# Kernel tuning notes

Measured on AMD Instinct MI355X. Metric: run time of the kernel, lower is better.

## Reference

```python
import jax, jax.numpy as jnp
import numpy as np

B, N, C_IN, G = 8, 65536, 16, 64
CH = [16, 16]
EPS = 1e-3  # keras BatchNormalization default epsilon
OFFSETS = [(dx, dy, dz) for dx in (-1, 0, 1) for dy in (-1, 0, 1) for dz in (-1, 0, 1)]
G3 = G * G * G


def setup_inputs() -> dict:
    key = jax.random.key(0)
    k = jax.random.split(key, 8)
    voxel_features = jax.random.normal(k[0], (B, N, C_IN), dtype=jnp.float32)
    # unique active voxel coordinates per example (submanifold sites)
    lin = jax.vmap(lambda kk: jax.random.permutation(kk, G3)[:N])(jax.random.split(k[1], B))
    xyz = jnp.stack([lin // (G * G), (lin // G) % G, lin % G], axis=-1).astype(jnp.int32)
    num_valid_voxels = jax.random.randint(k[2], (B,), N // 2, N + 1).astype(jnp.int32)
    w0 = jax.random.uniform(k[3], (3, 3, 3, C_IN, CH[0]), minval=-0.05, maxval=0.05, dtype=jnp.float32)
    w1 = jax.random.uniform(k[4], (3, 3, 3, CH[0], CH[1]), minval=-0.05, maxval=0.05, dtype=jnp.float32)
    nw0 = jax.random.uniform(k[5], (3, 3, 3, 1, 1), minval=-0.05, maxval=0.05, dtype=jnp.float32)
    nw1 = jax.random.uniform(k[6], (3, 3, 3, 1, 1), minval=-0.05, maxval=0.05, dtype=jnp.float32)
    gamma0 = jnp.ones((CH[0],), jnp.float32); beta0 = jnp.zeros((CH[0],), jnp.float32)
    gamma1 = jnp.ones((CH[1],), jnp.float32); beta1 = jnp.zeros((CH[1],), jnp.float32)
    return dict(voxel_features=voxel_features, voxel_xyz_indices=xyz,
                num_valid_voxels=num_valid_voxels, w0=w0, w1=w1, nw0=nw0, nw1=nw1,
                gamma0=gamma0, beta0=beta0, gamma1=gamma1, beta1=beta1)


def build_neighbor_idx(coords, valid_mask):
    """For each voxel and each 3x3x3 offset, the row index of the active neighbor, or -1."""
    lin = coords[..., 0] * (G * G) + coords[..., 1] * G + coords[..., 2]  # [B,N]
    # invalid (padded) voxels write to a spare slot so they never match as neighbors
    write_lin = jnp.where(valid_mask, lin, G3 + 1)
    idx_map = jnp.full((B, G3 + 2), -1, jnp.int32)
    idx_map = idx_map.at[jnp.arange(B)[:, None], write_lin].set(
        jnp.broadcast_to(jnp.arange(N, dtype=jnp.int32)[None, :], (B, N)))
    brow = jnp.arange(B)[:, None]
    nb = []
    for dx, dy, dz in OFFSETS:
        nx = coords[..., 0] + dx; ny = coords[..., 1] + dy; nz = coords[..., 2] + dz
        inb = (nx >= 0) & (nx < G) & (ny >= 0) & (ny < G) & (nz >= 0) & (nz < G)
        nlin = jnp.where(inb, nx * (G * G) + ny * G + nz, G3)  # slot G3 always -1
        nb.append(idx_map[brow, nlin])
    return jnp.stack(nb, axis=1)  # [B,27,N]


def sparse_conv(feats, nb_idx, valid_mask, w):
    """Submanifold sparse 3D conv: output only at active sites, gathering active neighbors."""
    wf = w.reshape(27, w.shape[3], w.shape[4])  # offsets enumerate kernel taps in order
    out = jnp.zeros((feats.shape[0], feats.shape[1], w.shape[4]), feats.dtype)
    for o in range(27):
        idx = nb_idx[:, o]  # [B,N]
        g = jnp.take_along_axis(feats, jnp.maximum(idx, 0)[..., None], axis=1)
        g = jnp.where((idx >= 0)[..., None], g, 0.0)
        out = out + jnp.einsum('bnc,co->bno', g, wf[o])
    return out * valid_mask[..., None]


def masked_bn(x, valid_mask, num_valid, gamma, beta):
    m = valid_mask[..., None].astype(x.dtype)
    cnt = jnp.sum(num_valid).astype(x.dtype)
    mean = jnp.sum(x * m, axis=(0, 1)) / cnt
    var = jnp.sum(m * jnp.square(x - mean), axis=(0, 1)) / cnt
    xn = (x - mean) * jax.lax.rsqrt(var + EPS) * gamma + beta
    return xn * m  # padded rows are zero-padded, as in the TF layer


def reference(voxel_features, voxel_xyz_indices, num_valid_voxels,
              w0, w1, nw0, nw1, gamma0, beta0, gamma1, beta1):
    valid_mask = jnp.arange(N)[None, :] < num_valid_voxels[:, None]  # [B,N]
    nb_idx = build_neighbor_idx(voxel_xyz_indices, valid_mask)
    ones = jnp.ones((B, N, 1), jnp.float32)
    net = voxel_features
    for w, nw, g, b in ((w0, nw0, gamma0, beta0), (w1, nw1, gamma1, beta1)):
        net = sparse_conv(net, nb_idx, valid_mask, w)
        net_norm = sparse_conv(ones, nb_idx, valid_mask, nw)
        net = net / (1.0 + jnp.abs(net_norm))
        net = masked_bn(net, valid_mask, num_valid_voxels, g, b)
        net = jax.nn.relu(net)
    return net
```

## Files before the change

### kernel.cpp

```cpp
#include <hip/hip_runtime.h>
#include <cstdint>
#include <cstddef>

#define NB 8
#define NN 65536
#define NS (NN + 16)
#define GG 64
#define GG3 (GG*GG*GG)
#define NW (GG3/32)
#define NBLKC 2048
#define NP32 (NB * 2048)
#define EPSC 1e-3f

typedef __bf16 bf16x8 __attribute__((ext_vector_type(8)));
typedef float  f32x4  __attribute__((ext_vector_type(4)));

__device__ __forceinline__ unsigned short f2bf(float f) {
    unsigned u = __builtin_bit_cast(unsigned, f);
    unsigned r = (u + 0x7fffu + ((u >> 16) & 1u)) >> 16;
    return (unsigned short)r;
}
__device__ __forceinline__ unsigned pk2(float a, float b) {
    return (unsigned)f2bf(a) | ((unsigned)f2bf(b) << 16);
}
__device__ __forceinline__ float bf2f(unsigned short s) {
    return __builtin_bit_cast(float, (unsigned)s << 16);
}

__device__ __forceinline__ int site_rank2(const int2* __restrict__ mwb, int lin) {
    int2 mw = mwb[lin >> 5];
    uint32_t w = (uint32_t)mw.x;
    uint32_t bit = 1u << (lin & 31);
    if (!(w & bit)) return -1;
    return mw.y + __popc(w & (bit - 1u));
}

__global__ __launch_bounds__(256) void build_mask_kernel(
    const int* __restrict__ xyz, const int* __restrict__ nvv,
    uint32_t* __restrict__ mask, int* __restrict__ linb,
    const float* __restrict__ w0, const float* __restrict__ w1,
    unsigned short* __restrict__ wf)
{
    int b = blockIdx.y;
    int n = blockIdx.x * 256 + threadIdx.x;
    if (n < nvv[b]) {
        const int* cp = xyz + ((size_t)b * NN + n) * 3;
        int lin = cp[0] * (GG * GG) + cp[1] * GG + cp[2];
        linb[(size_t)b * NN + n] = lin;
        atomicOr(&mask[b * NW + (lin >> 5)], 1u << (lin & 31));
    }
    if (blockIdx.x == 0 && b < 2) {
        const float* w = b ? w1 : w0;
        unsigned short* o = wf + b * 14 * 512;
        for (int idx = threadIdx.x; idx < 14 * 512; idx += 256) {
            int i = idx >> 9;
            int rem = idx & 511;
            int L = rem >> 3, j = rem & 7;
            int quad = L >> 4, nn = L & 15;
            int off = 2 * i + (quad >> 1);
            int c = ((quad & 1) << 3) + j;
            float v = (off < 27) ? w[(off * 16 + c) * 16 + nn] : 0.f;
            o[idx] = f2bf(v);
        }
    }
}

__global__ __launch_bounds__(256) void scan_mask_kernel(
    const uint32_t* __restrict__ mask, int2* __restrict__ mwb)
{
    int b = blockIdx.x;
    const uint32_t* mb = mask + (size_t)b * NW;
    int2* wb = mwb + (size_t)b * NW;
    int t = threadIdx.x;

    uint32_t wv[32];
    int cnts[32];
    int local = 0;
    #pragma unroll
    for (int i = 0; i < 32; i++) {
        wv[i] = mb[t * 32 + i];
        cnts[i] = __popc(wv[i]);
        local += cnts[i];
    }

    __shared__ int sc[256];
    sc[t] = local;
    __syncthreads();
    for (int off = 1; off < 256; off <<= 1) {
        int v = (t >= off) ? sc[t - off] : 0;
        __syncthreads();
        sc[t] += v;
        __syncthreads();
    }
    int base = sc[t] - local;
    #pragma unroll
    for (int i = 0; i < 32; i++) {
        wb[t * 32 + i] = make_int2((int)wv[i], base);
        base += cnts[i];
    }
}

__global__ __launch_bounds__(256) void perm_gather_kernel(
    const int* __restrict__ linb, const int* __restrict__ nvv,
    const int2* __restrict__ mwb,
    const float* __restrict__ feats,
    int2* __restrict__ srow,
    unsigned short* __restrict__ sfeats)
{
    int b = blockIdx.y;
    int n = blockIdx.x * 256 + threadIdx.x;
    int cnt = nvv[b];
    unsigned short* sfb = sfeats + (size_t)b * NS * 16;
    if (blockIdx.x == 0 && threadIdx.x < 16)
        sfb[(size_t)NN * 16 + threadIdx.x] = 0;
    if (n < cnt) {
        int lin = linb[(size_t)b * NN + n];
        int r = site_rank2(mwb + (size_t)b * NW, lin);
        srow[(size_t)b * NN + r] = make_int2(lin, n);
        const float4* fp = (const float4*)(feats + ((size_t)b * NN + n) * 16);
        float4 f0 = fp[0], f1 = fp[1], f2 = fp[2], f3 = fp[3];
        uint4 lo = make_uint4(pk2(f0.x, f0.y), pk2(f0.z, f0.w),
                              pk2(f1.x, f1.y), pk2(f1.z, f1.w));
        uint4 hi = make_uint4(pk2(f2.x, f2.y), pk2(f2.z, f2.w),
                              pk2(f3.x, f3.y), pk2(f3.z, f3.w));
        *(uint4*)(sfb + (size_t)r * 16)     = lo;
        *(uint4*)(sfb + (size_t)r * 16 + 8) = hi;
    }
}

__global__ __launch_bounds__(256, 4) void conv_mfma_kernel(
    const unsigned short* __restrict__ sfeats,
    const int2*     __restrict__ srow,
    const int*      __restrict__ nvv,
    const int2*     __restrict__ mwb,
    const unsigned short* __restrict__ wfrag,
    const float*    __restrict__ nw,
    unsigned short* __restrict__ outbuf,
    float*          __restrict__ stats)
{
    int lane = threadIdx.x & 63;
    int wv = threadIdx.x >> 6;
    int m = lane & 15, quad = lane >> 4;
    int v = lane & 31, h = lane >> 5;
    int wid = blockIdx.x * 4 + wv;

    __shared__ int   ubuf[4][32 * 29];
    __shared__ float rrl[4][32];
    __shared__ float red[4][32];
    __shared__ float lnw[27];
    int*   jj   = ubuf[wv];
    float* obuf = (float*)ubuf[wv];

    if (threadIdx.x < 27) lnw[threadIdx.x] = nw[threadIdx.x];

    bf16x8 bfr[14];
    #pragma unroll
    for (int i = 0; i < 14; i++)
        bfr[i] = *(const bf16x8*)(wfrag + i * 512 + lane * 8);
    __syncthreads();

    float psum = 0.f, psq = 0.f;
    int coff = (quad & 1) << 3;

    for (int pb = wid; pb < NP32; pb += 4 * NBLKC) {
        int b = pb >> 11;
        int r0 = (pb & 2047) << 5;
        int cnt = nvv[b];
        if (r0 >= cnt) continue;

        const int2* mb = mwb + (size_t)b * NW;
        const unsigned short* fb = sfeats + (size_t)b * NS * 16;
        const int2* sr = srow + (size_t)b * NN;

        int Rv = r0 + v;
        bool vld = Rv < cnt;
        int lin = vld ? sr[Rv].x : 0;
        int x = lin >> 12, y = (lin >> 6) & 63, z = lin & 63;
        int zb = z & 31;
        float nc = 0.f;
        #pragma unroll
        for (int t = 0; t < 5; t++) {
            int c = 2 * t + h;
            bool cok = c < 9;
            int cc = cok ? c : 0;
            int dx = cc / 3 - 1, dy = cc % 3 - 1;
            int nx = x + dx, ny = y + dy;
            bool colok = cok & ((unsigned)nx < 64u) & ((unsigned)ny < 64u);
            int wdi = colok ? (((nx << 12) + (ny << 6) + z) >> 5) : 0;

            int2 mw = make_int2(0, 0);
            if (vld & colok) mw = mb[wdi];
            bool need2 = vld & colok & (((zb == 0) & (z > 0)) | ((zb == 31) & (z < 63)));
            int w2 = wdi + ((zb == 0) ? -1 : 1);
            int2 mw2 = make_int2(0, 0);
            if (need2) mw2 = mb[w2];

            #pragma unroll
            for (int dz = -1; dz <= 1; dz++) {
                int zz = z + dz;
                bool zok = (unsigned)zz < 64u;
                bool same = (dz == 0) | ((dz < 0) ? (zb != 0) : (zb != 31));
                int2 word = same ? mw : mw2;
                int bb = zz & 31;
                uint32_t wm = (uint32_t)word.x;
                bool hit = vld & colok & zok & ((wm >> bb) & 1u);
                int rnk = word.y + __popc(wm & ((1u << bb) - 1u));
                int off = cc * 3 + dz + 1;
                int jv = hit ? rnk : NN;
                if (cok) {
                    jj[v * 29 + off] = jv;
                    nc += hit ? lnw[off] : 0.f;
                }
            }
        }
        nc += __shfl_xor(nc, 32, 64);
        if (lane < 32) rrl[wv][v] = 1.f / (1.f + fabsf(nc));

        f32x4 acc0 = {0.f, 0.f, 0.f, 0.f};
        f32x4 acc1 = {0.f, 0.f, 0.f, 0.f};
        #pragma unroll
        for (int i = 0; i < 14; i++) {
            int off = 2 * i + (quad >> 1);
            int idx = off < 27 ? off : 28;
            int j0 = jj[m * 29 + idx];        j0 = (off < 27) ? j0 : NN;
            int j1 = jj[(m + 16) * 29 + idx]; j1 = (off < 27) ? j1 : NN;
            bf16x8 a0 = *(const bf16x8*)(fb + (size_t)j0 * 16 + coff);
            bf16x8 a1 = *(const bf16x8*)(fb + (size_t)j1 * 16 + coff);
            acc0 = __builtin_amdgcn_mfma_f32_16x16x32_bf16(a0, bfr[i], acc0, 0, 0, 0);
            acc1 = __builtin_amdgcn_mfma_f32_16x16x32_bf16(a1, bfr[i], acc1, 0, 0, 0);
        }

        #pragma unroll
        for (int hh = 0; hh < 2; hh++) {
            #pragma unroll
            for (int r4 = 0; r4 < 4; r4++) {
                int row = (hh << 4) + (quad << 2) + r4;
                float tval = (hh ? acc1[r4] : acc0[r4]) * rrl[wv][row];
                psum += tval; psq += tval * tval;
                obuf[row * 17 + m] = tval;
            }
        }
        {
            int Rr = r0 + v;
            if (Rr < cnt) {
                const float* src = &obuf[v * 17 + h * 8];
                uint4 val = make_uint4(pk2(src[0], src[1]), pk2(src[2], src[3]),
                                       pk2(src[4], src[5]), pk2(src[6], src[7]));
                *(uint4*)(outbuf + ((size_t)b * NS + Rr) * 16 + h * 8) = val;
            }
        }
    }

    psum += __shfl_xor(psum, 16, 64); psum += __shfl_xor(psum, 32, 64);
    psq  += __shfl_xor(psq, 16, 64);  psq  += __shfl_xor(psq, 32, 64);
    if (lane < 16) { red[wv][lane] = psum; red[wv][16 + lane] = psq; }
    __syncthreads();
    if (threadIdx.x < 32) {
        float vv = red[0][threadIdx.x] + red[1][threadIdx.x] +
                   red[2][threadIdx.x] + red[3][threadIdx.x];
        atomicAdd(&stats[(blockIdx.x & 15) * 32 + threadIdx.x], vv);
    }
}

__device__ __forceinline__ void compute_sb(
    const float* __restrict__ stats, const int* __restrict__ nvv,
    const float* __restrict__ gamma, const float* __restrict__ beta,
    float* sbs , float* sums )
{
    int tid = threadIdx.x;
    if (tid < 32) {
        float v = 0.f;
        #pragma unroll
        for (int s = 0; s < 16; s++) v += stats[s * 32 + tid];
        sums[tid] = v;
    }
    __syncthreads();
    if (tid < 16) {
        float cnt = 0.f;
        #pragma unroll
        for (int b = 0; b < NB; b++) cnt += (float)nvv[b];
        float mean = sums[tid] / cnt;
        float var  = fmaxf(sums[16 + tid] / cnt - mean * mean, 0.f);
        float scv = gamma[tid] * rsqrtf(var + EPSC);
        sbs[tid]      = scv;
        sbs[16 + tid] = beta[tid] - mean * scv;
    }
    __syncthreads();
}

__global__ __launch_bounds__(256) void bnrelu_sorted_kernel(
    unsigned short* __restrict__ buf, const float* __restrict__ stats,
    const int* __restrict__ nvv,
    const float* __restrict__ gamma, const float* __restrict__ beta)
{
    __shared__ float sbs[32];
    __shared__ float sums[32];
    compute_sb(stats, nvv, gamma, beta, sbs, sums);

    int b = blockIdx.y;
    int r = blockIdx.x * 256 + threadIdx.x;
    if (r > NN) return;
    int cnt = nvv[b];
    unsigned short* op = buf + ((size_t)b * NS + r) * 16;
    if (r < cnt) {
        uint4 xl = *(const uint4*)op, xh = *(const uint4*)(op + 8);
        float y[16];
        #pragma unroll
        for (int c = 0; c < 16; c++) {
            unsigned u = (c < 8) ? ((const unsigned*)&xl)[c >> 1]
                                 : ((const unsigned*)&xh)[(c - 8) >> 1];
            unsigned short sv = (c & 1) ? (unsigned short)(u >> 16)
                                        : (unsigned short)(u & 0xffff);
            y[c] = fmaxf(fmaf(bf2f(sv), sbs[c], sbs[16 + c]), 0.f);
        }
        *(uint4*)op       = make_uint4(pk2(y[0], y[1]), pk2(y[2], y[3]),
                                       pk2(y[4], y[5]), pk2(y[6], y[7]));
        *(uint4*)(op + 8) = make_uint4(pk2(y[8], y[9]), pk2(y[10], y[11]),
                                       pk2(y[12], y[13]), pk2(y[14], y[15]));
    } else if (r == NN) {
        uint4 z = make_uint4(0, 0, 0, 0);
        *(uint4*)op       = z;
        *(uint4*)(op + 8) = z;
    }
}

__global__ __launch_bounds__(256) void final_scatter_kernel(
    const unsigned short* __restrict__ in,
    const int2* __restrict__ srow,
    const float* __restrict__ stats, const int* __restrict__ nvv,
    const float* __restrict__ gamma, const float* __restrict__ beta,
    float* __restrict__ out)
{
    __shared__ float sbs[32];
    __shared__ float sums[32];
    compute_sb(stats, nvv, gamma, beta, sbs, sums);

    int b = blockIdx.y;
    int r = blockIdx.x * 256 + threadIdx.x;
    int cnt = nvv[b];
    if (r < cnt) {
        const uint4* ip = (const uint4*)(in + ((size_t)b * NS + r) * 16);
        uint4 xl = ip[0], xh = ip[1];
        float y[16];
        #pragma unroll
        for (int c = 0; c < 16; c++) {
            unsigned u = (c < 8) ? ((const unsigned*)&xl)[c >> 1]
                                 : ((const unsigned*)&xh)[(c - 8) >> 1];
            unsigned short sv = (c & 1) ? (unsigned short)(u >> 16)
                                        : (unsigned short)(u & 0xffff);
            y[c] = fmaxf(fmaf(bf2f(sv), sbs[c], sbs[16 + c]), 0.f);
        }
        int n = srow[(size_t)b * NN + r].y;
        float4* op = (float4*)(out + ((size_t)b * NN + n) * 16);
        op[0] = make_float4(y[0],  y[1],  y[2],  y[3]);
        op[1] = make_float4(y[4],  y[5],  y[6],  y[7]);
        op[2] = make_float4(y[8],  y[9],  y[10], y[11]);
        op[3] = make_float4(y[12], y[13], y[14], y[15]);
    } else {
        float4 z = make_float4(0.f, 0.f, 0.f, 0.f);
        float4* op = (float4*)(out + ((size_t)b * NN + r) * 16);
        op[0] = z; op[1] = z; op[2] = z; op[3] = z;
    }
}

extern "C" void kernel_launch(void* const* d_in, const int* in_sizes, int n_in,
                              void* d_out, int out_size, void* d_ws, size_t ws_size,
                              hipStream_t stream)
{
    const float* feats  = (const float*)d_in[0];
    const int*   xyz    = (const int*)d_in[1];
    const int*   nvv    = (const int*)d_in[2];
    const float* w0     = (const float*)d_in[3];
    const float* w1     = (const float*)d_in[4];
    const float* nw0    = (const float*)d_in[5];
    const float* nw1    = (const float*)d_in[6];
    const float* gamma0 = (const float*)d_in[7];
    const float* beta0  = (const float*)d_in[8];
    const float* gamma1 = (const float*)d_in[9];
    const float* beta1  = (const float*)d_in[10];
    float* out = (float*)d_out;

    char* ws = (char*)d_ws;
    uint32_t* mask    = (uint32_t*)ws;       ws += (size_t)NB * NW * 4;
    float*    stats1  = (float*)ws;          ws += 16 * 32 * 4;
    float*    stats2  = (float*)ws;          ws += 16 * 32 * 4;
    int2*     mwb     = (int2*)ws;           ws += (size_t)NB * NW * 8;
    int2*     srow    = (int2*)ws;           ws += (size_t)NB * NN * 8;
    int*      linb    = (int*)ws;            ws += (size_t)NB * NN * 4;
    unsigned short* sfA = (unsigned short*)ws; ws += (size_t)NB * NS * 16 * 2;
    unsigned short* sfB = (unsigned short*)ws; ws += (size_t)NB * NS * 16 * 2;
    unsigned short* wfr = (unsigned short*)ws; ws += (size_t)2 * 14 * 512 * 2;

    hipMemsetAsync(mask, 0, (size_t)NB * NW * 4 + 16 * 32 * 4 * 2, stream);

    dim3 gridBN(NN / 256, NB);
    build_mask_kernel<<<gridBN, 256, 0, stream>>>(xyz, nvv, mask, linb, w0, w1, wfr);
    scan_mask_kernel<<<NB, 256, 0, stream>>>(mask, mwb);
    perm_gather_kernel<<<gridBN, 256, 0, stream>>>(linb, nvv, mwb, feats, srow, sfA);

    conv_mfma_kernel<<<NBLKC, 256, 0, stream>>>(
        sfA, srow, nvv, mwb, wfr, nw0, sfB, stats1);
    bnrelu_sorted_kernel<<<dim3(NN / 256 + 1, NB), 256, 0, stream>>>(
        sfB, stats1, nvv, gamma0, beta0);

    conv_mfma_kernel<<<NBLKC, 256, 0, stream>>>(
        sfB, srow, nvv, mwb, wfr + 14 * 512, nw1, sfA, stats2);

    final_scatter_kernel<<<dim3(NN / 256, NB), 256, 0, stream>>>(
        sfA, srow, stats2, nvv, gamma1, beta1, out);
}
```

Measured before the change: 242.0 us.

## Fuse first BN+ReLU into second conv gather and make final output a gather

Removes the standalone BN/ReLU pass over the sorted intermediate by applying the scale/bias and ReLU to each gathered neighbor row inside the second convolution, masking the sentinel zero row explicitly. The sorted-row table is split into a linear-coordinate array and an original-to-sorted index map, so the final kernel reads via gather and writes output coalesced instead of scattering. This trades a full memory pass and a launch for redundant per-neighbor ALU work (27x per row) in the conv inner loop.

Result: slower. 275.5 us (+13.8%).

```diff
diff --git a/kernel.cpp b/kernel.cpp
--- a/kernel.cpp
+++ b/kernel.cpp
@@ -104,7 +104,7 @@
     const int* __restrict__ linb, const int* __restrict__ nvv,
     const int2* __restrict__ mwb,
     const float* __restrict__ feats,
-    int2* __restrict__ srow,
+    int* __restrict__ slin, int* __restrict__ n2r,
     unsigned short* __restrict__ sfeats)
 {
     int b = blockIdx.y;
@@ -116,7 +116,8 @@
     if (n < cnt) {
         int lin = linb[(size_t)b * NN + n];
         int r = site_rank2(mwb + (size_t)b * NW, lin);
-        srow[(size_t)b * NN + r] = make_int2(lin, n);
+        slin[(size_t)b * NN + r] = lin;
+        n2r[(size_t)b * NN + n] = r;
         const float4* fp = (const float4*)(feats + ((size_t)b * NN + n) * 16);
         float4 f0 = fp[0], f1 = fp[1], f2 = fp[2], f3 = fp[3];
         uint4 lo = make_uint4(pk2(f0.x, f0.y), pk2(f0.z, f0.w),
@@ -128,13 +129,43 @@
     }
 }
 
+__device__ __forceinline__ void compute_sb(
+    const float* __restrict__ stats, const int* __restrict__ nvv,
+    const float* __restrict__ gamma, const float* __restrict__ beta,
+    float* sbs , float* sums )
+{
+    int tid = threadIdx.x;
+    if (tid < 32) {
+        float v = 0.f;
+        #pragma unroll
+        for (int s = 0; s < 16; s++) v += stats[s * 32 + tid];
+        sums[tid] = v;
+    }
+    __syncthreads();
+    if (tid < 16) {
+        float cnt = 0.f;
+        #pragma unroll
+        for (int b = 0; b < NB; b++) cnt += (float)nvv[b];
+        float mean = sums[tid] / cnt;
+        float var  = fmaxf(sums[16 + tid] / cnt - mean * mean, 0.f);
+        float scv = gamma[tid] * rsqrtf(var + EPSC);
+        sbs[tid]      = scv;
+        sbs[16 + tid] = beta[tid] - mean * scv;
+    }
+    __syncthreads();
+}
+
+template<bool FUSEBN>
 __global__ __launch_bounds__(256, 4) void conv_mfma_kernel(
     const unsigned short* __restrict__ sfeats,
-    const int2*     __restrict__ srow,
+    const int*      __restrict__ slin,
     const int*      __restrict__ nvv,
     const int2*     __restrict__ mwb,
     const unsigned short* __restrict__ wfrag,
     const float*    __restrict__ nw,
+    const float*    __restrict__ statsin,
+    const float*    __restrict__ gammain,
+    const float*    __restrict__ betain,
     unsigned short* __restrict__ outbuf,
     float*          __restrict__ stats)
 {
@@ -148,10 +179,23 @@
     __shared__ float rrl[4][32];
     __shared__ float red[4][32];
     __shared__ float lnw[27];
+    __shared__ float sbs[32];
+    __shared__ float sums[32];
     int*   jj   = ubuf[wv];
     float* obuf = (float*)ubuf[wv];
 
     if (threadIdx.x < 27) lnw[threadIdx.x] = nw[threadIdx.x];
+    if (FUSEBN) compute_sb(statsin, nvv, gammain, betain, sbs, sums);
+
+    int coff = (quad & 1) << 3;
+    float sc8[8], bi8[8];
+    if (FUSEBN) {
+        #pragma unroll
+        for (int k = 0; k < 8; k++) {
+            sc8[k] = sbs[coff + k];
+            bi8[k] = sbs[16 + coff + k];
+        }
+    }
 
     bf16x8 bfr[14];
     #pragma unroll
@@ -160,7 +204,6 @@
     __syncthreads();
 
     float psum = 0.f, psq = 0.f;
-    int coff = (quad & 1) << 3;
 
     for (int pb = wid; pb < NP32; pb += 4 * NBLKC) {
         int b = pb >> 11;
@@ -170,11 +213,11 @@
 
         const int2* mb = mwb + (size_t)b * NW;
         const unsigned short* fb = sfeats + (size_t)b * NS * 16;
-        const int2* sr = srow + (size_t)b * NN;
+        const int* sr = slin + (size_t)b * NN;
 
         int Rv = r0 + v;
         bool vld = Rv < cnt;
-        int lin = vld ? sr[Rv].x : 0;
+        int lin = vld ? sr[Rv] : 0;
         int x = lin >> 12, y = (lin >> 6) & 63, z = lin & 63;
         int zb = z & 31;
         float nc = 0.f;
@@ -226,6 +269,22 @@
             int j1 = jj[(m + 16) * 29 + idx]; j1 = (off < 27) ? j1 : NN;
             bf16x8 a0 = *(const bf16x8*)(fb + (size_t)j0 * 16 + coff);
             bf16x8 a1 = *(const bf16x8*)(fb + (size_t)j1 * 16 + coff);
+            if (FUSEBN) {
+                bf16x8 t0, t1;
+                #pragma unroll
+                for (int k = 0; k < 8; k++) {
+                    float y0 = fmaxf(fmaf((float)a0[k], sc8[k], bi8[k]), 0.f);
+                    float y1 = fmaxf(fmaf((float)a1[k], sc8[k], bi8[k]), 0.f);
+                    t0[k] = (__bf16)y0;
+                    t1[k] = (__bf16)y1;
+                }
+                uint4 u0 = __builtin_bit_cast(uint4, t0);
+                uint4 u1 = __builtin_bit_cast(uint4, t1);
+                if (j0 == NN) { u0 = make_uint4(0, 0, 0, 0); }
+                if (j1 == NN) { u1 = make_uint4(0, 0, 0, 0); }
+                a0 = __builtin_bit_cast(bf16x8, u0);
+                a1 = __builtin_bit_cast(bf16x8, u1);
+            }
             acc0 = __builtin_amdgcn_mfma_f32_16x16x32_bf16(a0, bfr[i], acc0, 0, 0, 0);
             acc1 = __builtin_amdgcn_mfma_f32_16x16x32_bf16(a1, bfr[i], acc1, 0, 0, 0);
         }
@@ -262,48 +321,25 @@
     }
 }
 
-__device__ __forceinline__ void compute_sb(
+__global__ __launch_bounds__(256) void final_gather_kernel(
+    const unsigned short* __restrict__ in,
+    const int* __restrict__ n2r,
     const float* __restrict__ stats, const int* __restrict__ nvv,
     const float* __restrict__ gamma, const float* __restrict__ beta,
-    float* sbs , float* sums )
-{
-    int tid = threadIdx.x;
-    if (tid < 32) {
-        float v = 0.f;
-        #pragma unroll
-        for (int s = 0; s < 16; s++) v += stats[s * 32 + tid];
-        sums[tid] = v;
-    }
-    __syncthreads();
-    if (tid < 16) {
-        float cnt = 0.f;
-        #pragma unroll
-        for (int b = 0; b < NB; b++) cnt += (float)nvv[b];
-        float mean = sums[tid] / cnt;
-        float var  = fmaxf(sums[16 + tid] / cnt - mean * mean, 0.f);
-        float scv = gamma[tid] * rsqrtf(var + EPSC);
-        sbs[tid]      = scv;
-        sbs[16 + tid] = beta[tid] - mean * scv;
-    }
-    __syncthreads();
-}
-
-__global__ __launch_bounds__(256) void bnrelu_sorted_kernel(
-    unsigned short* __restrict__ buf, const float* __restrict__ stats,
-    const int* __restrict__ nvv,
-    const float* __restrict__ gamma, const float* __restrict__ beta)
+    float* __restrict__ out)
 {
     __shared__ float sbs[32];
     __shared__ float sums[32];
     compute_sb(stats, nvv, gamma, beta, sbs, sums);
 
     int b = blockIdx.y;
-    int r = blockIdx.x * 256 + threadIdx.x;
-    if (r > NN) return;
+    int n = blockIdx.x * 256 + threadIdx.x;
     int cnt = nvv[b];
-    unsigned short* op = buf + ((size_t)b * NS + r) * 16;
-    if (r < cnt) {
-        uint4 xl = *(const uint4*)op, xh = *(const uint4*)(op + 8);
+    float4* op = (float4*)(out + ((size_t)b * NN + n) * 16);
+    if (n < cnt) {
+        int r = n2r[(size_t)b * NN + n];
+        const uint4* ip = (const uint4*)(in + ((size_t)b * NS + r) * 16);
+        uint4 xl = ip[0], xh = ip[1];
         float y[16];
         #pragma unroll
         for (int c = 0; c < 16; c++) {
@@ -313,52 +349,12 @@
                                         : (unsigned short)(u & 0xffff);
             y[c] = fmaxf(fmaf(bf2f(sv), sbs[c], sbs[16 + c]), 0.f);
         }
-        *(uint4*)op       = make_uint4(pk2(y[0], y[1]), pk2(y[2], y[3]),
-                                       pk2(y[4], y[5]), pk2(y[6], y[7]));
-        *(uint4*)(op + 8) = make_uint4(pk2(y[8], y[9]), pk2(y[10], y[11]),
-                                       pk2(y[12], y[13]), pk2(y[14], y[15]));
-    } else if (r == NN) {
-        uint4 z = make_uint4(0, 0, 0, 0);
-        *(uint4*)op       = z;
-        *(uint4*)(op + 8) = z;
-    }
-}
-
-__global__ __launch_bounds__(256) void final_scatter_kernel(
-    const unsigned short* __restrict__ in,
-    const int2* __restrict__ srow,
-    const float* __restrict__ stats, const int* __restrict__ nvv,
-    const float* __restrict__ gamma, const float* __restrict__ beta,
-    float* __restrict__ out)
-{
-    __shared__ float sbs[32];
-    __shared__ float sums[32];
-    compute_sb(stats, nvv, gamma, beta, sbs, sums);
-
-    int b = blockIdx.y;
-    int r = blockIdx.x * 256 + threadIdx.x;
-    int cnt = nvv[b];
-    if (r < cnt) {
-        const uint4* ip = (const uint4*)(in + ((size_t)b * NS + r) * 16);
-        uint4 xl = ip[0], xh = ip[1];
-        float y[16];
-        #pragma unroll
-        for (int c = 0; c < 16; c++) {
-            unsigned u = (c < 8) ? ((const unsigned*)&xl)[c >> 1]
-                                 : ((const unsigned*)&xh)[(c - 8) >> 1];
-            unsigned short sv = (c & 1) ? (unsigned short)(u >> 16)
-                                        : (unsigned short)(u & 0xffff);
-            y[c] = fmaxf(fmaf(bf2f(sv), sbs[c], sbs[16 + c]), 0.f);
-        }
-        int n = srow[(size_t)b * NN + r].y;
-        float4* op = (float4*)(out + ((size_t)b * NN + n) * 16);
         op[0] = make_float4(y[0],  y[1],  y[2],  y[3]);
         op[1] = make_float4(y[4],  y[5],  y[6],  y[7]);
         op[2] = make_float4(y[8],  y[9],  y[10], y[11]);
         op[3] = make_float4(y[12], y[13], y[14], y[15]);
     } else {
         float4 z = make_float4(0.f, 0.f, 0.f, 0.f);
-        float4* op = (float4*)(out + ((size_t)b * NN + r) * 16);
         op[0] = z; op[1] = z; op[2] = z; op[3] = z;
     }
 }
@@ -385,7 +381,8 @@
     float*    stats1  = (float*)ws;          ws += 16 * 32 * 4;
     float*    stats2  = (float*)ws;          ws += 16 * 32 * 4;
     int2*     mwb     = (int2*)ws;           ws += (size_t)NB * NW * 8;
-    int2*     srow    = (int2*)ws;           ws += (size_t)NB * NN * 8;
+    int*      slin    = (int*)ws;            ws += (size_t)NB * NN * 4;
+    int*      n2r     = (int*)ws;            ws += (size_t)NB * NN * 4;
     int*      linb    = (int*)ws;            ws += (size_t)NB * NN * 4;
     unsigned short* sfA = (unsigned short*)ws; ws += (size_t)NB * NS * 16 * 2;
     unsigned short* sfB = (unsigned short*)ws; ws += (size_t)NB * NS * 16 * 2;
@@ -396,16 +393,14 @@
     dim3 gridBN(NN / 256, NB);
     build_mask_kernel<<<gridBN, 256, 0, stream>>>(xyz, nvv, mask, linb, w0, w1, wfr);
     scan_mask_kernel<<<NB, 256, 0, stream>>>(mask, mwb);
-    perm_gather_kernel<<<gridBN, 256, 0, stream>>>(linb, nvv, mwb, feats, srow, sfA);
-
-    conv_mfma_kernel<<<NBLKC, 256, 0, stream>>>(
-        sfA, srow, nvv, mwb, wfr, nw0, sfB, stats1);
-    bnrelu_sorted_kernel<<<dim3(NN / 256 + 1, NB), 256, 0, stream>>>(
-        sfB, stats1, nvv, gamma0, beta0);
-
-    conv_mfma_kernel<<<NBLKC, 256, 0, stream>>>(
-        sfB, srow, nvv, mwb, wfr + 14 * 512, nw1, sfA, stats2);
-
-    final_scatter_kernel<<<dim3(NN / 256, NB), 256, 0, stream>>>(
-        sfA, srow, stats2, nvv, gamma1, beta1, out);
-}
+    perm_gather_kernel<<<gridBN, 256, 0, stream>>>(linb, nvv, mwb, feats, slin, n2r, sfA);
+
+    conv_mfma_kernel<false><<<NBLKC, 256, 0, stream>>>(
+        sfA, slin, nvv, mwb, wfr, nw0, nullptr, nullptr, nullptr, sfB, stats1);
+
+    conv_mfma_kernel<true><<<NBLKC, 256, 0, stream>>>(
+        sfB, slin, nvv, mwb, wfr + 14 * 512, nw1, stats1, gamma0, beta0, sfA, stats2);
+
+    final_gather_kernel<<<gridBN, 256, 0, stream>>>(
+        sfA, n2r, stats2, nvv, gamma1, beta1, out);
+}
```
